# Kernel tuning notes

Hardware: AMD Instinct MI355X
Metric: run time of the kernel (lower is better)

Reference implementation:

```python
import jax, jax.numpy as jnp
import numpy as np

B, S, D, H = 2, 2048, 1024, 16
DK = D // H  # 64
THETA = 10000.0
SCALE = 1.0 / np.sqrt(DK)


def _rope(t, pos):
    """Apply rotary embedding. t: [b,h,s,dk], pos: [b,s] int."""
    inv_freq = THETA ** (-jnp.arange(0, DK, 2, dtype=jnp.float32) / DK)  # [dk/2]
    ang = pos[:, None, :, None].astype(jnp.float32) * inv_freq  # [b,1,s,dk/2]
    cos, sin = jnp.cos(ang), jnp.sin(ang)
    t1, t2 = t[..., 0::2], t[..., 1::2]  # interleaved pairs
    rot = jnp.stack([t1 * cos - t2 * sin, t1 * sin + t2 * cos], axis=-1)
    return rot.reshape(t.shape)


def setup_inputs() -> dict:
    key = jax.random.key(0)
    ks = jax.random.split(key, 9)
    sc = 0.02
    x = jax.random.normal(ks[0], (B, S, D), jnp.float32)
    token_position = jnp.tile(jnp.arange(S, dtype=jnp.int32)[None, :], (B, 1))
    Wq = jax.random.normal(ks[1], (D, D), jnp.float32) * sc
    Wk = jax.random.normal(ks[2], (D, D), jnp.float32) * sc
    Wv = jax.random.normal(ks[3], (D, D), jnp.float32) * sc
    Wo = jax.random.normal(ks[4], (D, D), jnp.float32) * sc
    bq = jnp.zeros((D,), jnp.float32)
    bk = jnp.zeros((D,), jnp.float32)
    bv = jnp.zeros((D,), jnp.float32)
    bo = jnp.zeros((D,), jnp.float32)
    return {"x": x, "token_position": token_position,
            "Wq": Wq, "bq": bq, "Wk": Wk, "bk": bk,
            "Wv": Wv, "bv": bv, "Wo": Wo, "bo": bo}


def reference(x, token_position, Wq, bq, Wk, bk, Wv, bv, Wo, bo):
    b, s, d = x.shape
    # projections, split heads: [b,s,d] -> [b,h,s,dk]
    def heads(t):
        return t.reshape(b, s, H, DK).transpose(0, 2, 1, 3)
    q = heads(x @ Wq + bq)
    k = heads(x @ Wk + bk)
    v = heads(x @ Wv + bv)
    q = _rope(q, token_position)
    k = _rope(k, token_position)
    scores = jnp.einsum('bhnk,bhmk->bhnm', q, k) * SCALE  # [b,h,s,s]
    causal = jnp.tril(jnp.ones((s, s), dtype=bool))
    scores = jnp.where(causal, scores, -jnp.inf)
    probs = jax.nn.softmax(scores, axis=-1)
    o = jnp.einsum('bhnm,bhmk->bhnk', probs, v)  # [b,h,s,dk]
    o = o.transpose(0, 2, 1, 3).reshape(b, s, d)
    return o @ Wo + bo
```

## Files before the change

kernel.cpp:

```cpp
#include <hip/hip_runtime.h>
#include <math.h>

#define BB  2
#define SS  2048
#define DD  1024
#define HH  16
#define DKK 64

constexpr float kScale = 0.125f;
constexpr float kC1 = 0.18033688011112042f;
constexpr float kC2 = 23.0831206542234144f;

typedef __bf16 bf16x8 __attribute__((ext_vector_type(8)));
typedef __bf16 bf16x4 __attribute__((ext_vector_type(4)));
typedef float f32x4 __attribute__((ext_vector_type(4)));

__device__ __forceinline__ void async_copy16(const void* g, void* l) {
  __builtin_amdgcn_global_load_lds(
      (const __attribute__((address_space(1))) void*)g,
      (__attribute__((address_space(3))) void*)l, 16, 0, 0);
}

__global__ __launch_bounds__(256) void prep_kernel(
    const float* __restrict__ x, const int* __restrict__ pos,
    const float* __restrict__ W0, const float* __restrict__ W1,
    const float* __restrict__ W2, const float* __restrict__ W3,
    __bf16* __restrict__ xb, float2* __restrict__ rtab,
    __bf16* __restrict__ T0, __bf16* __restrict__ T1,
    __bf16* __restrict__ T2, __bf16* __restrict__ T3) {
  __shared__ __bf16 tile[64][65];
  const int bid = blockIdx.x;
  const int t = threadIdx.x;
  if (bid < 2048) {
    const size_t i = ((size_t)bid * 256 + t) * 8;
    const float4 v0 = *(const float4*)(x + i);
    const float4 v1 = *(const float4*)(x + i + 4);
    bf16x8 o;
    o[0] = (__bf16)v0.x; o[1] = (__bf16)v0.y; o[2] = (__bf16)v0.z; o[3] = (__bf16)v0.w;
    o[4] = (__bf16)v1.x; o[5] = (__bf16)v1.y; o[6] = (__bf16)v1.z; o[7] = (__bf16)v1.w;
    *(bf16x8*)(xb + i) = o;
  } else if (bid < 2560) {
    const int idx = (bid - 2048) * 256 + t;
    const int m = idx >> 5, pi = idx & 31;
    const float inv = exp2f(-0.4152410118609203f * (float)pi);
    float sn, cs;
    __sincosf((float)pos[m] * inv, &sn, &cs);
    rtab[idx] = make_float2(cs, sn);
  } else {
    const int tid2 = bid - 2560;
    const int z = tid2 >> 8, rem = tid2 & 255;
    const float* W;
    __bf16* T;
    switch (z) {
      case 0: W = W0; T = T0; break;
      case 1: W = W1; T = T1; break;
      case 2: W = W2; T = T2; break;
      default: W = W3; T = T3; break;
    }
    const int k0 = (rem >> 4) * 64, n0 = (rem & 15) * 64;
    const int c = t & 63, rg = t >> 6;
#pragma unroll
    for (int i = 0; i < 16; i++) {
      const int r = rg + i * 4;
      tile[r][c] = (__bf16)W[(size_t)(k0 + r) * DD + n0 + c];
    }
    __syncthreads();
#pragma unroll
    for (int i = 0; i < 16; i++) {
      const int r = rg + i * 4;
      T[(size_t)(n0 + r) * DD + k0 + c] = tile[c][r];
    }
  }
}

__device__ __forceinline__ void gemm_core(
    const __bf16* __restrict__ A, const __bf16* __restrict__ Bt,
    int bm, int bn, f32x4 (&acc)[4][4], __bf16* As, __bf16* Bs) {
  const int t = threadIdx.x;
  const int lane = t & 63, wave = t >> 6;
  const int col = lane & 15, quad = lane >> 4;
  const int wm = (wave & 1) * 64, wn = (wave >> 1) * 64;

  const int r16 = lane >> 2;
  const int gch = (lane & 3) ^ ((r16 >> 1) & 3);
  const __bf16* ag = A + (size_t)(bm + wave * 32 + r16) * DD + gch * 8;
  const __bf16* bg = Bt + (size_t)(bn + wave * 32 + r16) * DD + gch * 8;
  __bf16* asb = As + wave * 1024;
  __bf16* bsb = Bs + wave * 1024;

  const int rch = (quad ^ ((col >> 1) & 3)) * 8;

  auto stage = [&](int kt, int buf) {
    const int bo = buf * 4096;
    async_copy16(ag + kt, asb + bo);
    async_copy16(ag + (size_t)16 * DD + kt, asb + bo + 512);
    async_copy16(bg + kt, bsb + bo);
    async_copy16(bg + (size_t)16 * DD + kt, bsb + bo + 512);
  };

  stage(0, 0);
  stage(32, 1);

  int rb = 0, sb = 2;
#pragma unroll 1
  for (int step = 0; step < 32; step++) {
    if (step < 31)
      asm volatile("s_waitcnt vmcnt(4)" ::: "memory");
    else
      asm volatile("s_waitcnt vmcnt(0)" ::: "memory");
    __builtin_amdgcn_s_barrier();
    asm volatile("" ::: "memory");

    const int bo = rb * 4096;
    bf16x8 af[4], bf[4];
#pragma unroll
    for (int i = 0; i < 4; i++)
      af[i] = *(const bf16x8*)(As + bo + (wm + i * 16 + col) * 32 + rch);
#pragma unroll
    for (int j = 0; j < 4; j++)
      bf[j] = *(const bf16x8*)(Bs + bo + (wn + j * 16 + col) * 32 + rch);

    if (step + 2 < 32) stage((step + 2) * 32, sb);

    __builtin_amdgcn_s_setprio(1);
#pragma unroll
    for (int i = 0; i < 4; i++)
#pragma unroll
      for (int j = 0; j < 4; j++)
        acc[i][j] =
            __builtin_amdgcn_mfma_f32_16x16x32_bf16(af[i], bf[j], acc[i][j], 0, 0, 0);
    __builtin_amdgcn_s_setprio(0);

    rb = rb == 2 ? 0 : rb + 1;
    sb = sb == 2 ? 0 : sb + 1;
  }
}

__global__ __launch_bounds__(256, 3) void qkv_gemm_kernel(
    const __bf16* __restrict__ xb, const __bf16* __restrict__ WqT,
    const __bf16* __restrict__ WkT, const __bf16* __restrict__ WvT,
    const float* __restrict__ bq, const float* __restrict__ bk,
    const float* __restrict__ bv, const float2* __restrict__ ropetab,
    __bf16* __restrict__ qo, __bf16* __restrict__ ko, __bf16* __restrict__ vo) {
  __shared__ __bf16 As[3 * 128 * 32];
  __shared__ __bf16 Bs[3 * 128 * 32];
  const int mat = blockIdx.x >> 3;
  const int bn = (blockIdx.x & 7) * 128;
  const int bm = blockIdx.y * 128;

  f32x4 acc[4][4] = {};
  const int t = threadIdx.x, lane = t & 63, wave = t >> 6;
  const int col = lane & 15, quad = lane >> 4;
  const int wm = (wave & 1) * 64, wn = (wave >> 1) * 64;

  if (mat == 2) {
    gemm_core(WvT, xb, bn, bm, acc, As, Bs);
    const int b = bm >> 11;
#pragma unroll
    for (int i = 0; i < 4; i++) {
#pragma unroll
      for (int r = 0; r < 4; r++) {
        const int n = bn + wm + i * 16 + quad * 4 + r;
        const float bb = bv[n];
        const int h = n >> 6, dk = n & 63;
        __bf16* vrow = vo + ((size_t)(b * HH + h) * DKK + dk) * SS;
#pragma unroll
        for (int j = 0; j < 4; j++) {
          const int m = bm + wn + j * 16 + col;
          vrow[m & (SS - 1)] = (__bf16)(acc[i][j][r] + bb);
        }
      }
    }
    return;
  }

  const __bf16* Bt = mat == 0 ? WqT : WkT;
  const float* bias = mat == 0 ? bq : bk;
  __bf16* out = mat == 0 ? qo : ko;
  gemm_core(xb, Bt, bm, bn, acc, As, Bs);

#pragma unroll
  for (int i = 0; i < 4; i++) {
#pragma unroll
    for (int j = 0; j < 4; j++) {
      const int n = bn + wn + j * 16 + col;
      const float bb = bias[n];
      const int pi = (n & 63) >> 1;
#pragma unroll
      for (int r = 0; r < 4; r++) {
        const int m = bm + wm + i * 16 + quad * 4 + r;
        float v = acc[i][j][r] + bb;
        {
          const float other = __shfl_xor(v, 1, 64);
          const float2 cssn = ropetab[(size_t)m * 32 + pi];
          v = (n & 1) ? (other * cssn.y + v * cssn.x)
                      : (v * cssn.x - other * cssn.y);
        }
        const int h = n >> 6, dk = n & 63;
        const int b = m >> 11, s = m & (SS - 1);
        out[((size_t)(b * HH + h) * SS + s) * DKK + dk] = (__bf16)v;
      }
    }
  }
}

__global__ __launch_bounds__(256, 3) void oproj_gemm_kernel(
    const __bf16* __restrict__ ob, const __bf16* __restrict__ WoT,
    const float* __restrict__ bo, float* __restrict__ out) {
  __shared__ __bf16 As[3 * 128 * 32];
  __shared__ __bf16 Bs[3 * 128 * 32];
  const int bn = blockIdx.x * 128;
  const int bm = blockIdx.y * 128;
  f32x4 acc[4][4] = {};
  gemm_core(ob, WoT, bm, bn, acc, As, Bs);

  const int t = threadIdx.x, lane = t & 63, wave = t >> 6;
  const int col = lane & 15, quad = lane >> 4;
  const int wm = (wave & 1) * 64, wn = (wave >> 1) * 64;
#pragma unroll
  for (int i = 0; i < 4; i++) {
#pragma unroll
    for (int j = 0; j < 4; j++) {
      const int n = bn + wn + j * 16 + col;
      const float bb = bo[n];
#pragma unroll
      for (int r = 0; r < 4; r++) {
        const int m = bm + wm + i * 16 + quad * 4 + r;
        out[(size_t)m * DD + n] = acc[i][j][r] + bb;
      }
    }
  }
}

__global__ __launch_bounds__(512, 4) void flash_attn_mfma_kernel(
    const __bf16* __restrict__ q, const __bf16* __restrict__ k,
    const __bf16* __restrict__ vt, __bf16* __restrict__ o) {
  __shared__ __bf16 Ks[2][64 * 64];
  __shared__ __bf16 Vs[2][64 * 64];
  __shared__ __bf16 Ps[8][16 * 72];

  const int bh = blockIdx.x;
  const int qtile = 15 - blockIdx.y;
  const int t = threadIdx.x, lane = t & 63, wave = t >> 6;
  const int col = lane & 15, quad = lane >> 4;
  const int r8 = lane >> 3;
  const int cg = (lane & 7) ^ r8;
  const int w4 = wave & 3;

  const __bf16* qb = q + (size_t)bh * SS * DKK;
  const __bf16* kb = k + (size_t)bh * SS * DKK;
  const __bf16* vtb = vt + (size_t)bh * DKK * SS;
  const int b = bh / HH, h = bh % HH;
  __bf16* pw = (__bf16*)Ps[wave];

  const int rbase = qtile * 128 + wave * 16;
  const int myDiag = 2 * qtile + (wave >> 2);
  const int nTiles = 2 * qtile + 2;

  bf16x8 qf[2];
#pragma unroll
  for (int ks = 0; ks < 2; ks++)
    qf[ks] = *(const bf16x8*)(qb + (size_t)(rbase + col) * DKK + ks * 32 +
                              quad * 8);

  f32x4 oacc[4] = {};
  float l_lane = 0.f;

  auto stage = [&](int kt, int buf) {
    async_copy16(kb + (size_t)(kt * 64 + wave * 8 + r8) * DKK + cg * 8,
                 &Ks[buf][wave * 512]);
    async_copy16(vtb + (size_t)(wave * 8 + r8) * SS + kt * 64 + cg * 8,
                 &Vs[buf][wave * 512]);
  };

  stage(0, 0);
  __syncthreads();

  int cur = 0;
  for (int kt = 0; kt < nTiles; kt++) {
    if (kt + 1 < nTiles) stage(kt + 1, cur ^ 1);

    if (kt <= myDiag) {
      f32x4 sc[4] = {};
      __builtin_amdgcn_s_setprio(1);
#pragma unroll
      for (int ct = 0; ct < 4; ct++)
#pragma unroll
        for (int ks = 0; ks < 2; ks++) {
          const bf16x8 kf = *(const bf16x8*)(&Ks[cur][(ct * 16 + col) * 64 +
                                             (((ks * 4 + quad) ^ (col & 7)) * 8)]);
          sc[ct] = __builtin_amdgcn_mfma_f32_16x16x32_bf16(kf, qf[ks], sc[ct],
                                                           0, 0, 0);
        }
      __builtin_amdgcn_s_setprio(0);

      if (kt < myDiag) {
#pragma unroll
        for (int ct = 0; ct < 4; ct++) {
          float p0 = exp2f(sc[ct][0] * kC1 - kC2);
          float p1 = exp2f(sc[ct][1] * kC1 - kC2);
          float p2 = exp2f(sc[ct][2] * kC1 - kC2);
          float p3 = exp2f(sc[ct][3] * kC1 - kC2);
          l_lane += (p0 + p1) + (p2 + p3);
          bf16x4 pv;
          pv[0] = (__bf16)p0; pv[1] = (__bf16)p1;
          pv[2] = (__bf16)p2; pv[3] = (__bf16)p3;
          *(bf16x4*)(pw + col * 72 + ct * 16 + quad * 4) = pv;
        }
      } else {
#pragma unroll
        for (int ct = 0; ct < 4; ct++) {
          bf16x4 pv;
          if (ct > w4) {
            pv[0] = pv[1] = pv[2] = pv[3] = (__bf16)0.0f;
          } else if (ct < w4) {
            float p0 = exp2f(sc[ct][0] * kC1 - kC2);
            float p1 = exp2f(sc[ct][1] * kC1 - kC2);
            float p2 = exp2f(sc[ct][2] * kC1 - kC2);
            float p3 = exp2f(sc[ct][3] * kC1 - kC2);
            l_lane += (p0 + p1) + (p2 + p3);
            pv[0] = (__bf16)p0; pv[1] = (__bf16)p1;
            pv[2] = (__bf16)p2; pv[3] = (__bf16)p3;
          } else {
#pragma unroll
            for (int r = 0; r < 4; r++) {
              float p = exp2f(sc[ct][r] * kC1 - kC2);
              if (quad * 4 + r > col) p = 0.0f;
              l_lane += p;
              pv[r] = (__bf16)p;
            }
          }
          *(bf16x4*)(pw + col * 72 + ct * 16 + quad * 4) = pv;
        }
      }

      {
        bf16x8 pf[2];
#pragma unroll
        for (int ks = 0; ks < 2; ks++)
          pf[ks] = *(const bf16x8*)(pw + col * 72 + ks * 32 + quad * 8);
        __builtin_amdgcn_s_setprio(1);
#pragma unroll
        for (int dt = 0; dt < 4; dt++)
#pragma unroll
          for (int ks = 0; ks < 2; ks++) {
            const bf16x8 vf = *(const bf16x8*)(&Vs[cur][(dt * 16 + col) * 64 +
                                               (((ks * 4 + quad) ^ (col & 7)) * 8)]);
            oacc[dt] = __builtin_amdgcn_mfma_f32_16x16x32_bf16(pf[ks], vf,
                                                               oacc[dt], 0, 0, 0);
          }
        __builtin_amdgcn_s_setprio(0);
      }
    }

    __syncthreads();
    cur ^= 1;
  }

  float l = l_lane;
  l += __shfl_xor(l, 16, 64);
  l += __shfl_xor(l, 32, 64);
#pragma unroll
  for (int r = 0; r < 4; r++) {
    const float lr = __shfl(l, quad * 4 + r, 64);
    const float inv_l = 1.0f / lr;
    const int s = rbase + quad * 4 + r;
#pragma unroll
    for (int dt = 0; dt < 4; dt++)
      o[((size_t)(b * SS + s) * HH + h) * DKK + dt * 16 + col] =
          (__bf16)(oacc[dt][r] * inv_l);
  }
}

extern "C" void kernel_launch(void* const* d_in, const int* in_sizes, int n_in,
                              void* d_out, int out_size, void* d_ws,
                              size_t ws_size, hipStream_t stream) {
  const float* x  = (const float*)d_in[0];
  const int*  pos = (const int*)d_in[1];
  const float* Wq = (const float*)d_in[2];
  const float* bq = (const float*)d_in[3];
  const float* Wk = (const float*)d_in[4];
  const float* bk = (const float*)d_in[5];
  const float* Wv = (const float*)d_in[6];
  const float* bv = (const float*)d_in[7];
  const float* Wo = (const float*)d_in[8];
  const float* bo = (const float*)d_in[9];
  float* out = (float*)d_out;

  char* ws = (char*)d_ws;
  __bf16* xb  = (__bf16*)(ws);
  __bf16* WqT = (__bf16*)(ws + ((size_t)8  << 20));
  __bf16* WkT = (__bf16*)(ws + ((size_t)10 << 20));
  __bf16* WvT = (__bf16*)(ws + ((size_t)12 << 20));
  __bf16* WoT = (__bf16*)(ws + ((size_t)14 << 20));
  __bf16* qb  = (__bf16*)(ws + ((size_t)16 << 20));
  __bf16* kb  = (__bf16*)(ws + ((size_t)24 << 20));
  __bf16* vtb = (__bf16*)(ws + ((size_t)32 << 20));
  __bf16* ob  = (__bf16*)(ws + ((size_t)40 << 20));
  float2* rtab = (float2*)(ws + ((size_t)48 << 20));

  prep_kernel<<<3584, 256, 0, stream>>>(x, pos, Wq, Wk, Wv, Wo, xb, rtab, WqT,
                                        WkT, WvT, WoT);
  qkv_gemm_kernel<<<dim3(24, 32), 256, 0, stream>>>(xb, WqT, WkT, WvT, bq, bk,
                                                    bv, rtab, qb, kb, vtb);
  flash_attn_mfma_kernel<<<dim3(32, 16), 512, 0, stream>>>(qb, kb, vtb, ob);
  oproj_gemm_kernel<<<dim3(8, 32), 256, 0, stream>>>(ob, WoT, bo, out);
}
```

Before: 192.0 us.

## Split long causal query tiles across two KV halves and add combine kernel

The seven longest query tiles (qtiles 9–15) per batch-head are each split into two blocks that process the lower and upper halves of their KV range. Each half writes unnormalized fp32 partial outputs and row sums to workspace, and a new combine kernel adds the halves and normalizes them into the bf16 attention output. The aim is to even out per-block work in the causal attention grid, so that the longest tiles no longer set the tail latency. The costs are an extra kernel launch, an extra round trip of fp32 partials through global memory, and a tighter register budget from raising the occupancy hint in launch_bounds from 4 to 6, which could cause spills.

```diff
diff --git a/kernel.cpp b/kernel.cpp
--- a/kernel.cpp
+++ b/kernel.cpp
@@ -232,15 +232,32 @@
   }
 }
 
-__global__ __launch_bounds__(512, 4) void flash_attn_mfma_kernel(
+__global__ __launch_bounds__(512, 6) void flash_attn_mfma_kernel(
     const __bf16* __restrict__ q, const __bf16* __restrict__ k,
-    const __bf16* __restrict__ vt, __bf16* __restrict__ o) {
+    const __bf16* __restrict__ vt, __bf16* __restrict__ o,
+    float* __restrict__ Opart, float* __restrict__ lpart) {
   __shared__ __bf16 Ks[2][64 * 64];
   __shared__ __bf16 Vs[2][64 * 64];
   __shared__ __bf16 Ps[8][16 * 72];
 
   const int bh = blockIdx.x;
-  const int qtile = 15 - blockIdx.y;
+  const int y = blockIdx.y;
+  int qtile, ktBeg, ktEnd, half;
+  bool isSplit;
+  if (y < 14) {
+    qtile = 15 - (y >> 1);
+    half = y & 1;
+    isSplit = true;
+    ktBeg = half ? (qtile + 1) : 0;
+    ktEnd = half ? (2 * qtile + 2) : (qtile + 1);
+  } else {
+    qtile = 22 - y;
+    half = 0;
+    isSplit = false;
+    ktBeg = 0;
+    ktEnd = 2 * qtile + 2;
+  }
+
   const int t = threadIdx.x, lane = t & 63, wave = t >> 6;
   const int col = lane & 15, quad = lane >> 4;
   const int r8 = lane >> 3;
@@ -255,7 +272,6 @@
 
   const int rbase = qtile * 128 + wave * 16;
   const int myDiag = 2 * qtile + (wave >> 2);
-  const int nTiles = 2 * qtile + 2;
 
   bf16x8 qf[2];
 #pragma unroll
@@ -273,12 +289,12 @@
                  &Vs[buf][wave * 512]);
   };
 
-  stage(0, 0);
+  stage(ktBeg, 0);
   __syncthreads();
 
   int cur = 0;
-  for (int kt = 0; kt < nTiles; kt++) {
-    if (kt + 1 < nTiles) stage(kt + 1, cur ^ 1);
+  for (int kt = ktBeg; kt < ktEnd; kt++) {
+    if (kt + 1 < ktEnd) stage(kt + 1, cur ^ 1);
 
     if (kt <= myDiag) {
       f32x4 sc[4] = {};
@@ -360,15 +376,55 @@
   float l = l_lane;
   l += __shfl_xor(l, 16, 64);
   l += __shfl_xor(l, 32, 64);
-#pragma unroll
-  for (int r = 0; r < 4; r++) {
-    const float lr = __shfl(l, quad * 4 + r, 64);
-    const float inv_l = 1.0f / lr;
-    const int s = rbase + quad * 4 + r;
-#pragma unroll
-    for (int dt = 0; dt < 4; dt++)
-      o[((size_t)(b * SS + s) * HH + h) * DKK + dt * 16 + col] =
-          (__bf16)(oacc[dt][r] * inv_l);
+
+  if (!isSplit) {
+#pragma unroll
+    for (int r = 0; r < 4; r++) {
+      const float lr = __shfl(l, quad * 4 + r, 64);
+      const float inv_l = 1.0f / lr;
+      const int s = rbase + quad * 4 + r;
+#pragma unroll
+      for (int dt = 0; dt < 4; dt++)
+        o[((size_t)(b * SS + s) * HH + h) * DKK + dt * 16 + col] =
+            (__bf16)(oacc[dt][r] * inv_l);
+    }
+  } else {
+    const int tile = (bh * 7 + (qtile - 9)) * 2 + half;
+    float* Op = Opart + (size_t)tile * (128 * 64);
+#pragma unroll
+    for (int r = 0; r < 4; r++) {
+      const int row = wave * 16 + quad * 4 + r;
+#pragma unroll
+      for (int dt = 0; dt < 4; dt++)
+        Op[row * 64 + dt * 16 + col] = oacc[dt][r];
+    }
+    if (quad == 0) lpart[tile * 128 + wave * 16 + col] = l;
+  }
+}
+
+__global__ __launch_bounds__(256) void combine_kernel(
+    const float* __restrict__ Opart, const float* __restrict__ lpart,
+    __bf16* __restrict__ o) {
+  const int bh = blockIdx.x / 7, qi = blockIdx.x % 7;
+  const int qtile = qi + 9;
+  const int b = bh / HH, h = bh % HH;
+  const int t = threadIdx.x;
+  const int row = t >> 1, dk0 = (t & 1) * 32;
+  const int ta = (bh * 7 + qi) * 2, tb = ta + 1;
+  const float la = lpart[ta * 128 + row], lb = lpart[tb * 128 + row];
+  const float inv = 1.0f / (la + lb);
+  const int s = qtile * 128 + row;
+  const float* Oa = Opart + (size_t)ta * 8192 + row * 64 + dk0;
+  const float* Ob = Opart + (size_t)tb * 8192 + row * 64 + dk0;
+  __bf16* orow = o + ((size_t)(b * SS + s) * HH + h) * DKK + dk0;
+#pragma unroll
+  for (int i = 0; i < 32; i += 4) {
+    const float4 a = *(const float4*)(Oa + i);
+    const float4 bb = *(const float4*)(Ob + i);
+    orow[i + 0] = (__bf16)((a.x + bb.x) * inv);
+    orow[i + 1] = (__bf16)((a.y + bb.y) * inv);
+    orow[i + 2] = (__bf16)((a.z + bb.z) * inv);
+    orow[i + 3] = (__bf16)((a.w + bb.w) * inv);
   }
 }
 
@@ -398,11 +454,15 @@
   __bf16* vtb = (__bf16*)(ws + ((size_t)32 << 20));
   __bf16* ob  = (__bf16*)(ws + ((size_t)40 << 20));
   float2* rtab = (float2*)(ws + ((size_t)48 << 20));
+  float* Opart = (float*)(ws);
+  float* lpart = (float*)(ws + ((size_t)48 << 20));
 
   prep_kernel<<<3584, 256, 0, stream>>>(x, pos, Wq, Wk, Wv, Wo, xb, rtab, WqT,
                                         WkT, WvT, WoT);
   qkv_gemm_kernel<<<dim3(24, 32), 256, 0, stream>>>(xb, WqT, WkT, WvT, bq, bk,
                                                     bv, rtab, qb, kb, vtb);
-  flash_attn_mfma_kernel<<<dim3(32, 16), 512, 0, stream>>>(qb, kb, vtb, ob);
+  flash_attn_mfma_kernel<<<dim3(32, 23), 512, 0, stream>>>(qb, kb, vtb, ob,
+                                                           Opart, lpart);
+  combine_kernel<<<224, 256, 0, stream>>>(Opart, lpart, ob);
   oproj_gemm_kernel<<<dim3(8, 32), 256, 0, stream>>>(ob, WoT, bo, out);
 }
```

Result: no change. 191.8 us, median of 2 (-0.1%).
